# Optimization experiments

Measured on AMD Instinct MI355X. Metric: run time of the kernel, lower is better.

## Reference

```python
import jax, jax.numpy as jnp
import numpy as np

# model constants
D = 2048; D_INNER = 4096; H = 64; P = 64; N = 128; K = 4; CHUNK = 256
E = 8; TOPK = 2; I_EXP = 1024; I_SH = 4096
EPS = 1e-5; RES_MULT = 0.22
CONV_DIM = D_INNER + 2 * N  # n_groups=1


def rmsnorm(x, w, eps=EPS):
    var = jnp.mean(x * x, axis=-1, keepdims=True)
    return x * jax.lax.rsqrt(var + eps) * w


def segsum(x):
    # x: [..., L] -> [..., L, L] lower-triangular cumulative sums, -inf above diag
    L = x.shape[-1]
    cs = jnp.cumsum(x, axis=-1)
    d = cs[..., :, None] - cs[..., None, :]
    mask = jnp.tril(jnp.ones((L, L), dtype=bool))
    return jnp.where(mask, d, -jnp.inf)


def ssd(x, dt, A, Bm, Cm, chunk=CHUNK):
    # x:[b,s,h,p] dt:[b,s,h] A:[h] Bm/Cm:[b,s,n] (single group)
    b, S, h, p = x.shape
    n = Bm.shape[-1]
    nc = S // chunk
    xc = x.reshape(b, nc, chunk, h, p)
    dtc = dt.reshape(b, nc, chunk, h)
    Bc = Bm.reshape(b, nc, chunk, n)
    Cc = Cm.reshape(b, nc, chunk, n)
    dA = jnp.transpose(dtc * A, (0, 1, 3, 2))          # [b,c,h,l]
    dA_cum = jnp.cumsum(dA, axis=-1)                    # [b,c,h,l]
    xdt = xc * dtc[..., None]                           # [b,c,l,h,p]
    # intra-chunk (quadratic attention-like block)
    CB = jnp.einsum('bcln,bcsn->bcls', Cc, Bc)
    Lmat = jnp.exp(segsum(dA))                          # [b,c,h,l,s]
    Y = jnp.einsum('bcls,bchls,bcshp->bclhp', CB, Lmat, xdt)
    # per-chunk final states
    decay_states = jnp.exp(dA_cum[..., -1:] - dA_cum)   # [b,c,h,l]
    states = jnp.einsum('bcln,bchl,bclhp->bchpn', Bc, decay_states, xdt)
    # inter-chunk recurrence (small scan over nc chunks)
    chunk_decay = jnp.exp(dA_cum[..., -1])              # [b,c,h]
    dec_c = jnp.moveaxis(chunk_decay, 1, 0)             # [c,b,h]
    st_c = jnp.moveaxis(states, 1, 0)                   # [c,b,h,p,n]

    def step(carry, inp):
        dec, st = inp
        return carry * dec[..., None, None] + st, carry

    _, prev = jax.lax.scan(step, jnp.zeros_like(st_c[0]), (dec_c, st_c))
    prev = jnp.moveaxis(prev, 0, 1)                     # [b,c,h,p,n] state before each chunk
    out_decay = jnp.exp(jnp.transpose(dA_cum, (0, 1, 3, 2)))  # [b,c,l,h]
    Y = Y + jnp.einsum('bcln,bchpn->bclhp', Cc, prev) * out_decay[..., None]
    return Y.reshape(b, S, h, p)


def causal_conv_silu(u, w, bias):
    # u:[b,s,c], depthwise causal conv kernel w:[c,K]
    S = u.shape[1]
    up = jnp.pad(u, ((0, 0), (K - 1, 0), (0, 0)))
    y = sum(up[:, i:i + S, :] * w[:, i] for i in range(K)) + bias
    return jax.nn.silu(y)


def setup_inputs() -> dict:
    key = jax.random.key(0)
    ks = jax.random.split(key, 16)
    B, S = 1, 4096
    sc = 0.02
    return {
        'positions': jnp.arange(B * S, dtype=jnp.int32).reshape(B, S),
        'hidden_states': jax.random.normal(ks[0], (B, S, D), jnp.float32),
        'ln1_w': jnp.ones((D,), jnp.float32),
        'in_proj_w': jax.random.normal(ks[1], (D, 2 * D_INNER + 2 * N + H), jnp.float32) * sc,
        'conv_w': jax.random.normal(ks[2], (CONV_DIM, K), jnp.float32) * 0.2,
        'conv_b': jnp.zeros((CONV_DIM,), jnp.float32),
        'A_log': jnp.log(jax.random.uniform(ks[3], (H,), jnp.float32, 1.0, 16.0)),
        'dt_bias': jax.random.normal(ks[4], (H,), jnp.float32) * 0.5,
        'D_param': jnp.ones((H,), jnp.float32),
        'mamba_norm_w': jnp.ones((D_INNER,), jnp.float32),
        'out_proj_w': jax.random.normal(ks[5], (D_INNER, D), jnp.float32) * sc,
        'ln2_w': jnp.ones((D,), jnp.float32),
        'router_w': jax.random.normal(ks[6], (D, E), jnp.float32) * sc,
        'moe_w_gate_up': jax.random.normal(ks[7], (E, D, 2 * I_EXP), jnp.float32) * sc,
        'moe_w_down': jax.random.normal(ks[8], (E, I_EXP, D), jnp.float32) * sc,
        'shared_w_in': jax.random.normal(ks[9], (D, 2 * I_SH), jnp.float32) * sc,
        'shared_w_out': jax.random.normal(ks[10], (I_SH, D), jnp.float32) * sc,
    }


def reference(positions, hidden_states, ln1_w, in_proj_w, conv_w, conv_b, A_log,
              dt_bias, D_param, mamba_norm_w, out_proj_w, ln2_w, router_w,
              moe_w_gate_up, moe_w_down, shared_w_in, shared_w_out):
    B, S, _ = hidden_states.shape
    residual = hidden_states
    h = rmsnorm(hidden_states, ln1_w)
    # ---- Mamba2 mixer ----
    proj = h @ in_proj_w                                  # [B,S,2*Di+2N+H]
    z = proj[..., :D_INNER]
    xBC = proj[..., D_INNER:D_INNER + CONV_DIM]
    dt_raw = proj[..., D_INNER + CONV_DIM:]
    xBC = causal_conv_silu(xBC, conv_w, conv_b)
    x = xBC[..., :D_INNER].reshape(B, S, H, P)
    Bm = xBC[..., D_INNER:D_INNER + N]
    Cm = xBC[..., D_INNER + N:]
    dt = jax.nn.softplus(dt_raw + dt_bias)                # [B,S,H]
    A = -jnp.exp(A_log)                                   # [H]
    y = ssd(x, dt, A, Bm, Cm) + x * D_param[None, None, :, None]
    y = y.reshape(B, S, D_INNER)
    y = rmsnorm(y * jax.nn.silu(z), mamba_norm_w)         # gated RMSNorm
    mamba_out = y @ out_proj_w
    hidden = residual + mamba_out * RES_MULT
    residual = hidden
    # ---- MoE + shared MLP ----
    h2 = rmsnorm(hidden, ln2_w)
    ht = h2.reshape(-1, D)
    T = ht.shape[0]
    logits = ht @ router_w                                # [T,E]
    topv, topi = jax.lax.top_k(logits, TOPK)
    wts = jax.nn.softmax(topv, axis=-1)
    gates = jnp.zeros((T, E), ht.dtype).at[jnp.arange(T)[:, None], topi].set(wts)
    moe_out = jnp.zeros_like(ht)
    for e in range(E):
        gu = ht @ moe_w_gate_up[e]
        a = jax.nn.silu(gu[:, :I_EXP]) * gu[:, I_EXP:]
        moe_out = moe_out + gates[:, e:e + 1] * (a @ moe_w_down[e])
    gu = ht @ shared_w_in
    shared_out = (jax.nn.silu(gu[:, :I_SH]) * gu[:, I_SH:]) @ shared_w_out
    ff = (moe_out + shared_out).reshape(B, S, D)
    hidden = residual + ff * RES_MULT
    return (hidden, residual)
```

## Files before the change

### kernel.cpp

```cpp
#include <hip/hip_runtime.h>
#include <stdint.h>

typedef unsigned short u16;
typedef __attribute__((ext_vector_type(8))) __bf16 bf16x8;
typedef __attribute__((ext_vector_type(4))) float f32x4;

#define SEQ     4096
#define DMODEL  2048
#define DINNER  4096
#define NHEADS  64
#define HEADP   64
#define NSTATE  128
#define NCHUNK  16
#define CHUNKL  256
#define NPROJ   8512
#define NPROJP  8576
#define CONVDIM 4352
#define RESM    0.22f
#define MAXROWS 9216
#define MAXTILE 72

static __device__ __forceinline__ u16 f2bf(float f){
  union { float f; uint32_t u; } v; v.f = f;
  uint32_t r = v.u + 0x7fffu + ((v.u >> 16) & 1u);
  return (u16)(r >> 16);
}
static __device__ __forceinline__ float bf2f(u16 h){
  union { uint32_t u; float f; } v; v.u = ((uint32_t)h) << 16;
  return v.f;
}
static __device__ __forceinline__ float siluf(float x){ return x / (1.f + __expf(-x)); }

static __device__ __forceinline__ void gll16(const void* g, void* l) {
  __builtin_amdgcn_global_load_lds(
      (const __attribute__((address_space(1))) void*)g,
      (__attribute__((address_space(3))) void*)l, 16, 0, 0);
}

static __device__ __forceinline__ int swz_src_c8(int tid) {
  return ((((tid & 3) - ((tid >> 3) & 3) + 4) & 3) * 8);
}
static __device__ __forceinline__ int swz_rd_sl8(int fr, int g) {
  return (((g + ((fr >> 1) & 3)) & 3) * 8);
}

static __device__ __forceinline__ void decode_tile(
    int id, int NB, int MB, int G, int& bx, int& by)
{
  const int nwg = NB * MB;
  int sid = id;
  if (!(nwg & 7)) {
    const int cpx = nwg >> 3;
    sid = (id & 7) * cpx + (id >> 3);
  }
  const int gsz = MB * G;
  const int fullG = NB / G;
  const int fullCnt = fullG * gsz;
  if (sid < fullCnt) {
    const int grp = sid / gsz;
    const int r = sid - grp * gsz;
    const int q = r / G;
    by = q;
    bx = grp * G + (r - q * G);
  } else {
    const int rem = NB - fullG * G;
    const int r = sid - fullCnt;
    const int q = r / rem;
    by = q;
    bx = fullG * G + (r - q * rem);
  }
}

__global__ __launch_bounds__(256) void rmsnorm_split(
    const float* __restrict__ in, const float* __restrict__ w,
    u16* __restrict__ hi, u16* __restrict__ lo, int width)
{
  const int row = blockIdx.x;
  const float* x = in + (size_t)row * width;
  float ss = 0.f;
  for (int i = threadIdx.x * 4; i < width; i += 1024) {
    float4 v = *(const float4*)&x[i];
    ss += v.x*v.x + v.y*v.y + v.z*v.z + v.w*v.w;
  }
  #pragma unroll
  for (int off = 32; off > 0; off >>= 1) ss += __shfl_down(ss, off);
  __shared__ float red[4];
  if ((threadIdx.x & 63) == 0) red[threadIdx.x >> 6] = ss;
  __syncthreads();
// ... 128 lines not shown
        Cf[(size_t)m * ldc + n] = acc[mi][ni][i];
      }
    }
  }
}

__global__ __launch_bounds__(256, 2) void gemm_bt_glu(
    const u16* __restrict__ A, const u16* __restrict__ Bt,
    u16* __restrict__ aout,
    int K, int Nhalf, int NB, int MB, int G)
{
  __shared__ u16 As[128 * 32];
  __shared__ u16 Bs[128 * 32];
  int bx, by; decode_tile(blockIdx.x, NB, MB, G, bx, by);
  const int tid = threadIdx.x, lane = tid & 63;
  const int wid = tid >> 6, wr = wid >> 1, wc = wid & 1;
  const int m0 = by * 128, n0 = bx * 128;
  const int fr = lane & 15, g = lane >> 4;
  const int sl8 = swz_rd_sl8(fr, g);
  const f32x4 zero = {0.f, 0.f, 0.f, 0.f};
  f32x4 acc[4][4];
  #pragma unroll
  for (int i = 0; i < 4; i++)
    #pragma unroll
    for (int j = 0; j < 4; j++) acc[i][j] = zero;
  const int c8 = swz_src_c8(tid);
  const u16* pA = A  + (size_t)(m0 + (tid >> 2)) * K + c8;
  const u16* pB = Bt + (size_t)(n0 + (tid >> 2)) * K + c8;
  const size_t rstep = (size_t)64 * K;
  const int l0 = tid * 8;
  for (int k0 = 0; k0 < K; k0 += 32) {
    if (k0) __syncthreads();
    gll16(pA + k0,         &As[l0]);
    gll16(pA + k0 + rstep, &As[2048 + l0]);
    gll16(pB + k0,         &Bs[l0]);
    gll16(pB + k0 + rstep, &Bs[2048 + l0]);
    __syncthreads();
    bf16x8 af[4], bfr[4];
    #pragma unroll
    for (int mi = 0; mi < 4; mi++)
      af[mi] = *(const bf16x8*)&As[(wr * 64 + mi * 16 + fr) * 32 + sl8];
    #pragma unroll
    for (int ni = 0; ni < 4; ni++)
      bfr[ni] = *(const bf16x8*)&Bs[(wc * 64 + ni * 16 + fr) * 32 + sl8];
    #pragma unroll
    for (int mi = 0; mi < 4; mi++)
      #pragma unroll
      for (int ni = 0; ni < 4; ni++)
        acc[mi][ni] = __builtin_amdgcn_mfma_f32_16x16x32_bf16(af[mi], bfr[ni], acc[mi][ni], 0, 0, 0);
  }
  #pragma unroll
  for (int mi = 0; mi < 4; mi++) {
    #pragma unroll
    for (int ni = 0; ni < 4; ni++) {
      const int n = n0 + wc * 64 + ni * 16 + fr;
      #pragma unroll
      for (int i = 0; i < 4; i++) {
        const float v = acc[mi][ni][i];
        const float vp = __shfl_xor(v, 1);
        if (!(fr & 1)) {
          const int m = m0 + wr * 64 + mi * 16 + g * 4 + i;
          aout[(size_t)m * Nhalf + (n >> 1)] = f2bf(siluf(v) * vp);
        }
      }
    }
  }
}

template<int EPI>
__global__ __launch_bounds__(256, 2) void gemm_dd(
    const u16* __restrict__ Ah, const u16* __restrict__ Al,
    const u16* __restrict__ Bh, const u16* __restrict__ Bl,
    float* __restrict__ Cf, const float* __restrict__ res,
    int Nreal, int K, int ldc, float alpha, int NB, int MB, int G)
{
  __shared__ u16 Ash[128 * 32];
  __shared__ u16 Asl[128 * 32];
  __shared__ u16 Bsh[128 * 32];
  __shared__ u16 Bsl[128 * 32];
  int bx, by; decode_tile(blockIdx.x, NB, MB, G, bx, by);
  const int tid = threadIdx.x, lane = tid & 63;
  const int wid = tid >> 6, wr = wid >> 1, wc = wid & 1;
  const int m0 = by * 128, n0 = bx * 128;
  const int fr = lane & 15, g = lane >> 4;
  const int sl8 = swz_rd_sl8(fr, g);
  const f32x4 zero = {0.f, 0.f, 0.f, 0.f};
  f32x4 acc[4][4];
  #pragma unroll
  for (int i = 0; i < 4; i++)
    #pragma unroll
    for (int j = 0; j < 4; j++) acc[i][j] = zero;
  const int c8 = swz_src_c8(tid);
  const size_t offA = (size_t)(m0 + (tid >> 2)) * K + c8;
  const size_t offB = (size_t)(n0 + (tid >> 2)) * K + c8;
  const size_t rstep = (size_t)64 * K;
  const int l0 = tid * 8;
  for (int k0 = 0; k0 < K; k0 += 32) {
    if (k0) __syncthreads();
    gll16(Ah + offA + k0,         &Ash[l0]);
    gll16(Ah + offA + k0 + rstep, &Ash[2048 + l0]);
    gll16(Al + offA + k0,         &Asl[l0]);
    gll16(Al + offA + k0 + rstep, &Asl[2048 + l0]);
    gll16(Bh + offB + k0,         &Bsh[l0]);
    gll16(Bh + offB + k0 + rstep, &Bsh[2048 + l0]);
    gll16(Bl + offB + k0,         &Bsl[l0]);
    gll16(Bl + offB + k0 + rstep, &Bsl[2048 + l0]);
    __syncthreads();
    bf16x8 ah[4], al[4], bh[4], bl[4];
    #pragma unroll
    for (int mi = 0; mi < 4; mi++) {
      const int a = (wr * 64 + mi * 16 + fr) * 32 + sl8;
      ah[mi] = *(const bf16x8*)&Ash[a];
      al[mi] = *(const bf16x8*)&Asl[a];
    }
    #pragma unroll
    for (int ni = 0; ni < 4; ni++) {
      const int b = (wc * 64 + ni * 16 + fr) * 32 + sl8;
      bh[ni] = *(const bf16x8*)&Bsh[b];
      bl[ni] = *(const bf16x8*)&Bsl[b];
    }
    #pragma unroll
    for (int mi = 0; mi < 4; mi++)
      #pragma unroll
      for (int ni = 0; ni < 4; ni++) {
        acc[mi][ni] = __builtin_amdgcn_mfma_f32_16x16x32_bf16(al[mi], bh[ni], acc[mi][ni], 0, 0, 0);
        acc[mi][ni] = __builtin_amdgcn_mfma_f32_16x16x32_bf16(ah[mi], bl[ni], acc[mi][ni], 0, 0, 0);
        acc[mi][ni] = __builtin_amdgcn_mfma_f32_16x16x32_bf16(ah[mi], bh[ni], acc[mi][ni], 0, 0, 0);
      }
  }
  #pragma unroll
  for (int mi = 0; mi < 4; mi++) {
    #pragma unroll
    for (int ni = 0; ni < 4; ni++) {
      const int n = n0 + wc * 64 + ni * 16 + fr;
      if (n >= Nreal) continue;
      #pragma unroll
      for (int i = 0; i < 4; i++) {
        const int m = m0 + wr * 64 + mi * 16 + g * 4 + i;
        const float v = acc[mi][ni][i];
        const size_t idx = (size_t)m * ldc + n;
        if constexpr (EPI == 1) {
          Cf[idx] = res[idx] + alpha * v;
        } else {
          Cf[idx] = v;
        }
      }
    }
  }
}

__global__ __launch_bounds__(256, 2) void gemm_moe_gu(
    const u16* __restrict__ ht, const u16* __restrict__ wGU,
    u16* __restrict__ abufp, const int* __restrict__ tokmap,
    const int* __restrict__ meta)
{
  const int by = blockIdx.y;
  if (by >= meta[24]) return;
  const int e = meta[32 + by];
  const int row0 = meta[104 + by];
  __shared__ u16 As[128 * 32];
  __shared__ u16 Bs[128 * 32];
  const int tid = threadIdx.x, lane = tid & 63;
  const int wid = tid >> 6, wr = wid >> 1, wc = wid & 1;
  const int n0 = blockIdx.x * 128;
  const int fr = lane & 15, g = lane >> 4;
  const int sl8 = swz_rd_sl8(fr, g);
  const f32x4 zero = {0.f, 0.f, 0.f, 0.f};
  f32x4 acc[4][4];
  #pragma unroll
  for (int i = 0; i < 4; i++)
    #pragma unroll
    for (int j = 0; j < 4; j++) acc[i][j] = zero;
  const int r4 = tid >> 2, c8 = swz_src_c8(tid);
  const int tok0 = tokmap[row0 + r4];
  const int tok1 = tokmap[row0 + 64 + r4];
  const u16* pA0 = ht + (size_t)tok0 * DMODEL + c8;
  const u16* pA1 = ht + (size_t)tok1 * DMODEL + c8;
  const u16* pB  = wGU + (size_t)e * 2048 * DMODEL + (size_t)(n0 + r4) * DMODEL + c8;
  const size_t rstep = (size_t)64 * DMODEL;
  const int l0 = tid * 8;
  for (int k0 = 0; k0 < DMODEL; k0 += 32) {
    if (k0) __syncthreads();
    gll16(pA0 + k0,        &As[l0]);
    gll16(pA1 + k0,        &As[2048 + l0]);
    gll16(pB + k0,         &Bs[l0]);
    gll16(pB + k0 + rstep, &Bs[2048 + l0]);
    __syncthreads();
    bf16x8 af[4], bfr[4];
    #pragma unroll
    for (int mi = 0; mi < 4; mi++)
      af[mi] = *(const bf16x8*)&As[(wr * 64 + mi * 16 + fr) * 32 + sl8];
    #pragma unroll
    for (int ni = 0; ni < 4; ni++)
      bfr[ni] = *(const bf16x8*)&Bs[(wc * 64 + ni * 16 + fr) * 32 + sl8];
    #pragma unroll
    for (int mi = 0; mi < 4; mi++)
      #pragma unroll
      for (int ni = 0; ni < 4; ni++)
        acc[mi][ni] = __builtin_amdgcn_mfma_f32_16x16x32_bf16(af[mi], bfr[ni], acc[mi][ni], 0, 0, 0);
  }
  #pragma unroll
  for (int mi = 0; mi < 4; mi++)
    #pragma unroll
    for (int ni = 0; ni < 4; ni++) {
      const int n = n0 + wc * 64 + ni * 16 + fr;
      #pragma unroll
      for (int i = 0; i < 4; i++) {
        const float v = acc[mi][ni][i];
        const float vp = __shfl_xor(v, 1);
        if (!(fr & 1)) {
          const int m = row0 + wr * 64 + mi * 16 + g * 4 + i;
          abufp[(size_t)m * 1024 + (n >> 1)] = f2bf(siluf(v) * vp);
        }
      }
    }
}

__global__ __launch_bounds__(256, 2) void gemm_moe_down(
    const u16* __restrict__ abuf, const u16* __restrict__ wDN,
    u16* __restrict__ dout, const float* __restrict__ gatew,
    const int* __restrict__ meta)
{
  const int by = blockIdx.y;
  if (by >= meta[24]) return;
  const int e = meta[32 + by];
  const int row0 = meta[104 + by];
  __shared__ u16 As[128 * 32];
  __shared__ u16 Bs[128 * 32];
  const int tid = threadIdx.x, lane = tid & 63;
  const int wid = tid >> 6, wr = wid >> 1, wc = wid & 1;
  const int n0 = blockIdx.x * 128;
// ... 45 lines not shown

__global__ __launch_bounds__(256) void conv_silu_dt(
    const float* __restrict__ proj, const float* __restrict__ cw, const float* __restrict__ cb,
    const float* __restrict__ dt_bias,
    float* __restrict__ x, float* __restrict__ Bc, float* __restrict__ Cc,
    float* __restrict__ dt)
{
  const int c = blockIdx.x * 256 + threadIdx.x;
  const int s = blockIdx.y;
  if (c < CONVDIM) {
    const float4 w = *(const float4*)&cw[c * 4];
    float acc = cb[c];
    const float* pc = proj + (size_t)DINNER + c;
    if (s >= 3) acc += pc[(size_t)(s-3) * NPROJP] * w.x;
    if (s >= 2) acc += pc[(size_t)(s-2) * NPROJP] * w.y;
    if (s >= 1) acc += pc[(size_t)(s-1) * NPROJP] * w.z;
    acc += pc[(size_t)s * NPROJP] * w.w;
    const float v = siluf(acc);
    if (c < DINNER)                 x[(size_t)s * DINNER + c] = v;
    else if (c < DINNER + NSTATE)   Bc[(size_t)s * NSTATE + (c - DINNER)] = v;
    else                            Cc[(size_t)s * NSTATE + (c - DINNER - NSTATE)] = v;
  } else if (c < CONVDIM + 64) {
    const int h = c - CONVDIM;
    const float v = proj[(size_t)s * NPROJP + (DINNER + CONVDIM) + h] + dt_bias[h];
    dt[(size_t)s * 64 + h] = fmaxf(v, 0.f) + log1pf(__expf(-fabsf(v)));
  }
}

__global__ __launch_bounds__(64) void ssd_cum_seq(
    const float* __restrict__ dt, const float* __restrict__ A_log,
    float* __restrict__ cum, float* __restrict__ cdec)
{
  const int c = blockIdx.x, h = threadIdx.x;
  const float A = -__expf(A_log[h]);
  float run = 0.f;
  float* co = cum + ((size_t)(c * 64 + h)) * 256;
  const float* dp = dt + (size_t)c * 256 * 64 + h;
  #pragma unroll 4
  for (int l = 0; l < 256; l++) {
    run += dp[(size_t)l * 64] * A;
    co[l] = run;
  }
  cdec[c * 64 + h] = __expf(run);
}

__global__ __launch_bounds__(256) void ssd_cb(
    const float* __restrict__ Cc, const float* __restrict__ Bc, float* __restrict__ CBt)
{
  const int c = blockIdx.y;
  const int lt = blockIdx.x >> 2, st = blockIdx.x & 3;
  if (st > lt) return;
  __shared__ float Cn[128][64];
  __shared__ float Bn[128][64];
  const int tid = threadIdx.x;
  #pragma unroll
  for (int rep = 0; rep < 8; rep++) {
    const int lin = rep * 1024 + tid * 4;
    const int r = lin >> 7, cc = lin & 127;
    float4 cv = *(const float4*)&Cc[((size_t)(c*256 + lt*64 + r)) * 128 + cc];
    float4 bv = *(const float4*)&Bc[((size_t)(c*256 + st*64 + r)) * 128 + cc];
    Cn[cc+0][r] = cv.x; Cn[cc+1][r] = cv.y; Cn[cc+2][r] = cv.z; Cn[cc+3][r] = cv.w;
    Bn[cc+0][r] = bv.x; Bn[cc+1][r] = bv.y; Bn[cc+2][r] = bv.z; Bn[cc+3][r] = bv.w;
  }
  __syncthreads();
  const int lb = (tid >> 4) * 4, sb = (tid & 15) * 4;
  float acc[4][4] = {};
  for (int n = 0; n < 128; n++) {
    float cv[4], bv[4];
    #pragma unroll
    for (int i = 0; i < 4; i++) { cv[i] = Cn[n][lb+i]; bv[i] = Bn[n][sb+i]; }
    #pragma unroll
    for (int i = 0; i < 4; i++)
      #pragma unroll
      for (int j = 0; j < 4; j++) acc[i][j] += cv[i] * bv[j];
  }
  #pragma unroll
  for (int is = 0; is < 4; is++) {
    const int sg = st*64 + sb + is;
    float4 o; o.x = acc[0][is]; o.y = acc[1][is]; o.z = acc[2][is]; o.w = acc[3][is];
    *(float4*)&CBt[((size_t)(c*256 + sg)) * 256 + lt*64 + lb] = o;
  }
}

__global__ __launch_bounds__(256, 2) void ssd_intra_mfma(
    const float* __restrict__ x, const float* __restrict__ dt, const float* __restrict__ cum,
    const float* __restrict__ CBt, float* __restrict__ Yw)
{
  const int c = blockIdx.x, h = blockIdx.y;
  const int tid = threadIdx.x, lane = tid & 63, w = tid >> 6;
  const int fr = lane & 15, g = lane >> 4;
  __shared__ float cumL[256];
  __shared__ u16 Ph[256 * 32], Pl[256 * 32];
  __shared__ u16 Xh[64 * 32],  Xl[64 * 32];
  cumL[tid] = cum[((size_t)(c*64 + h)) * 256 + tid];
  const f32x4 zero = {0.f, 0.f, 0.f, 0.f};
  f32x4 acc[4][4];
  #pragma unroll
  for (int i = 0; i < 4; i++)
    #pragma unroll
    for (int j = 0; j < 4; j++) acc[i][j] = zero;
  const size_t cb0 = (size_t)c * 65536;
  for (int ts = 0; ts < 8; ts++) {
    __syncthreads();
    {
      const int sl = tid >> 3, p0 = (tid & 7) * 8;
      const int sg = c*256 + ts*32 + sl;
      const float dtv = dt[(size_t)sg * 64 + h];
      const float* xr = x + (size_t)sg * DINNER + h*64 + p0;
      const float4 v0 = *(const float4*)&xr[0];
      const float4 v1 = *(const float4*)&xr[4];
      #pragma unroll
      for (int q = 0; q < 8; q++) {
        const float v = ((q < 4) ? ((const float*)&v0)[q] : ((const float*)&v1)[q-4]) * dtv;
        const u16 H = f2bf(v);
        Xh[(p0 + q) * 32 + sl] = H;
        Xl[(p0 + q) * 32 + sl] = f2bf(v - bf2f(H));
      }
    }
    {
      const int l = tid;
      const float myc = cumL[l];
      #pragma unroll 4
      for (int j = 0; j < 32; j++) {
        const int s = ts*32 + j;
        const float cb = CBt[cb0 + (size_t)s * 256 + l];
        float p = 0.f;
        if (s <= l) p = cb * __expf(myc - cumL[s]);
        const u16 H = f2bf(p);
        Ph[l * 32 + j] = H;
        Pl[l * 32 + j] = f2bf(p - bf2f(H));
      }
    }
    __syncthreads();
    if (ts * 32 < (w + 1) * 64) {
      bf16x8 ah[4], al[4], bh[4], bl[4];
      #pragma unroll
      for (int mi = 0; mi < 4; mi++) {
        const int a = (w*64 + mi*16 + fr) * 32 + g*8;
        ah[mi] = *(const bf16x8*)&Ph[a];
        al[mi] = *(const bf16x8*)&Pl[a];
      }
      #pragma unroll
      for (int ni = 0; ni < 4; ni++) {
        const int b = (ni*16 + fr) * 32 + g*8;
        bh[ni] = *(const bf16x8*)&Xh[b];
        bl[ni] = *(const bf16x8*)&Xl[b];
      }
      #pragma unroll
      for (int mi = 0; mi < 4; mi++)
        #pragma unroll
        for (int ni = 0; ni < 4; ni++) {
          acc[mi][ni] = __builtin_amdgcn_mfma_f32_16x16x32_bf16(al[mi], bh[ni], acc[mi][ni], 0, 0, 0);
          acc[mi][ni] = __builtin_amdgcn_mfma_f32_16x16x32_bf16(ah[mi], bl[ni], acc[mi][ni], 0, 0, 0);
          acc[mi][ni] = __builtin_amdgcn_mfma_f32_16x16x32_bf16(ah[mi], bh[ni], acc[mi][ni], 0, 0, 0);
        }
    }
  }
  #pragma unroll
  for (int mi = 0; mi < 4; mi++)
    #pragma unroll
    for (int ni = 0; ni < 4; ni++)
      #pragma unroll
      for (int i = 0; i < 4; i++) {
        const int l = w*64 + mi*16 + g*4 + i;
        const int p = ni*16 + fr;
        Yw[(size_t)(c*256 + l) * DINNER + h*64 + p] = acc[mi][ni][i];
      }
}

__global__ __launch_bounds__(256, 2) void ssd_states_mfma(
    const float* __restrict__ x, const float* __restrict__ Bc, const float* __restrict__ dt,
    const float* __restrict__ cum, float* __restrict__ states)
{
  const int c = blockIdx.x, h = blockIdx.y;
  const int tid = threadIdx.x, lane = tid & 63, w = tid >> 6;
  const int fr = lane & 15, g = lane >> 4;
  __shared__ float cd[256];
  __shared__ u16 Xth[64 * 32],  Xtl[64 * 32];
  __shared__ u16 Bth[128 * 32], Btl[128 * 32];
  {
    const float* cumh = cum + ((size_t)(c*64 + h)) * 256;
    cd[tid] = __expf(cumh[255] - cumh[tid]) * dt[(size_t)(c*256 + tid) * 64 + h];
  }
  const f32x4 zero = {0.f, 0.f, 0.f, 0.f};
  f32x4 acc[4][2];
  #pragma unroll
  for (int i = 0; i < 4; i++) { acc[i][0] = zero; acc[i][1] = zero; }
  for (int lt = 0; lt < 8; lt++) {
    __syncthreads();
    {
      const int ll = tid >> 3, p0 = (tid & 7) * 8;
      const int lg = c*256 + lt*32 + ll;
      const float cdv = cd[lt*32 + ll];
      const float* xr = x + (size_t)lg * DINNER + h*64 + p0;
      const float4 v0 = *(const float4*)&xr[0];
      const float4 v1 = *(const float4*)&xr[4];
      #pragma unroll
      for (int q = 0; q < 8; q++) {
        const float v = ((q < 4) ? ((const float*)&v0)[q] : ((const float*)&v1)[q-4]) * cdv;
        const u16 H = f2bf(v);
        Xth[(p0 + q) * 32 + ll] = H;
        Xtl[(p0 + q) * 32 + ll] = f2bf(v - bf2f(H));
      }
    }
    {
      const int ll = tid >> 3, n0 = (tid & 7) * 16;
      const float* br = Bc + (size_t)(c*256 + lt*32 + ll) * 128 + n0;
      #pragma unroll
      for (int q4 = 0; q4 < 4; q4++) {
        const float4 bv = *(const float4*)&br[q4*4];
        #pragma unroll
        for (int q = 0; q < 4; q++) {
          const float v = ((const float*)&bv)[q];
          const u16 H = f2bf(v);
          Bth[(n0 + q4*4 + q) * 32 + ll] = H;
          Btl[(n0 + q4*4 + q) * 32 + ll] = f2bf(v - bf2f(H));
        }
      }
    }
    __syncthreads();
    bf16x8 ah[4], al[4], bh[2], bl[2];
    #pragma unroll
    for (int mi = 0; mi < 4; mi++) {
      const int a = (mi*16 + fr) * 32 + g*8;
      ah[mi] = *(const bf16x8*)&Xth[a];
      al[mi] = *(const bf16x8*)&Xtl[a];
    }
    #pragma unroll
    for (int ni = 0; ni < 2; ni++) {
      const int b = (w*32 + ni*16 + fr) * 32 + g*8;
      bh[ni] = *(const bf16x8*)&Bth[b];
      bl[ni] = *(const bf16x8*)&Btl[b];
    }
    #pragma unroll
    for (int mi = 0; mi < 4; mi++)
      #pragma unroll
      for (int ni = 0; ni < 2; ni++) {
        acc[mi][ni] = __builtin_amdgcn_mfma_f32_16x16x32_bf16(al[mi], bh[ni], acc[mi][ni], 0, 0, 0);
        acc[mi][ni] = __builtin_amdgcn_mfma_f32_16x16x32_bf16(ah[mi], bl[ni], acc[mi][ni], 0, 0, 0);
        acc[mi][ni] = __builtin_amdgcn_mfma_f32_16x16x32_bf16(ah[mi], bh[ni], acc[mi][ni], 0, 0, 0);
      }
  }
  #pragma unroll
  for (int mi = 0; mi < 4; mi++)
    #pragma unroll
    for (int ni = 0; ni < 2; ni++)
      #pragma unroll
      for (int i = 0; i < 4; i++) {
        const int p = mi*16 + g*4 + i;
        const int n = w*32 + ni*16 + fr;
        states[(((size_t)(c*64 + h)) * 64 + p) * 128 + n] = acc[mi][ni][i];
      }
}

__global__ void ssd_scan(
    const float* __restrict__ states, const float* __restrict__ cdec, float* __restrict__ prev)
{
  const int hp = blockIdx.x;
  const int n = threadIdx.x;
  const int h = hp >> 6;
  float carry = 0.f;
  for (int c = 0; c < NCHUNK; c++) {
    const size_t idx = ((size_t)c * 4096 + hp) * 128 + n;
    prev[idx] = carry;
    carry = carry * cdec[c*64 + h] + states[idx];
  }
}

__global__ __launch_bounds__(256, 2) void ssd_final_mfma(
    const float* __restrict__ Cc, const float* __restrict__ prev, const float* __restrict__ cum,
    const float* __restrict__ x, const float* __restrict__ proj, const float* __restrict__ Dp,
    float* __restrict__ Yw)
{
  const int c = blockIdx.x, h = blockIdx.y;
  const int tid = threadIdx.x, lane = tid & 63, w = tid >> 6;
  const int fr = lane & 15, g = lane >> 4;
  __shared__ float cumL[256];
  __shared__ u16 Ch[256 * 32], Cl[256 * 32];
  __shared__ u16 Pvh[64 * 32], Pvl[64 * 32];
  cumL[tid] = cum[((size_t)(c*64 + h)) * 256 + tid];
  const f32x4 zero = {0.f, 0.f, 0.f, 0.f};
  f32x4 acc[4][4];
  #pragma unroll
  for (int i = 0; i < 4; i++)
    #pragma unroll
    for (int j = 0; j < 4; j++) acc[i][j] = zero;
  for (int nt = 0; nt < 4; nt++) {
    __syncthreads();
    {
      #pragma unroll
      for (int rep = 0; rep < 32; rep++) {
        const int l = rep*8 + (tid >> 5);
        const int j = tid & 31;
        const float v = Cc[(size_t)(c*256 + l) * 128 + nt*32 + j];
        const u16 H = f2bf(v);
        Ch[l*32 + j] = H;
        Cl[l*32 + j] = f2bf(v - bf2f(H));
      }
    }
    {
      const int p = tid >> 2, q0 = (tid & 3) * 8;
      const float* pr = prev + ((size_t)c * 4096 + h*64 + p) * 128 + nt*32 + q0;
      const float4 v0 = *(const float4*)&pr[0];
      const float4 v1 = *(const float4*)&pr[4];
      #pragma unroll
      for (int q = 0; q < 8; q++) {
        const float v = (q < 4) ? ((const float*)&v0)[q] : ((const float*)&v1)[q-4];
        const u16 H = f2bf(v);
        Pvh[p*32 + q0 + q] = H;
        Pvl[p*32 + q0 + q] = f2bf(v - bf2f(H));
      }
    }
    __syncthreads();
    bf16x8 ah[4], al[4], bh[4], bl[4];
    #pragma unroll
    for (int mi = 0; mi < 4; mi++) {
      const int a = (w*64 + mi*16 + fr) * 32 + g*8;
      ah[mi] = *(const bf16x8*)&Ch[a];
      al[mi] = *(const bf16x8*)&Cl[a];
    }
    #pragma unroll
    for (int ni = 0; ni < 4; ni++) {
      const int b = (ni*16 + fr) * 32 + g*8;
      bh[ni] = *(const bf16x8*)&Pvh[b];
      bl[ni] = *(const bf16x8*)&Pvl[b];
    }
    #pragma unroll
    for (int mi = 0; mi < 4; mi++)
      #pragma unroll
      for (int ni = 0; ni < 4; ni++) {
        acc[mi][ni] = __builtin_amdgcn_mfma_f32_16x16x32_bf16(al[mi], bh[ni], acc[mi][ni], 0, 0, 0);
        acc[mi][ni] = __builtin_amdgcn_mfma_f32_16x16x32_bf16(ah[mi], bl[ni], acc[mi][ni], 0, 0, 0);
        acc[mi][ni] = __builtin_amdgcn_mfma_f32_16x16x32_bf16(ah[mi], bh[ni], acc[mi][ni], 0, 0, 0);
      }
  }
  const float Dv = Dp[h];
  #pragma unroll
  for (int mi = 0; mi < 4; mi++) {
    #pragma unroll
    for (int i = 0; i < 4; i++) {
      const int l = w*64 + mi*16 + g*4 + i;
      const float odec = __expf(cumL[l]);
      const size_t rowo = (size_t)(c*256 + l);
      #pragma unroll
      for (int ni = 0; ni < 4; ni++) {
        const int p = ni*16 + fr;
        const size_t iy = rowo * DINNER + h*64 + p;
        const float yv = Yw[iy] + acc[mi][ni][i] * odec + Dv * x[iy];
        const float z = proj[rowo * NPROJP + h*64 + p];
        Yw[iy] = yv * siluf(z);
      }
    }
  }
}

__global__ __launch_bounds__(256) void router_norm(
    const float* __restrict__ h2, const float* __restrict__ ln2w,
    const float* __restrict__ rw, u16* __restrict__ ht,
    int* __restrict__ eidx, float* __restrict__ ew)
{
  const int t = blockIdx.x;
  const float* xr = h2 + (size_t)t * DMODEL;
  float ss = 0.f;
  for (int i = threadIdx.x * 4; i < DMODEL; i += 1024) {
    float4 v = *(const float4*)&xr[i];
    ss += v.x*v.x + v.y*v.y + v.z*v.z + v.w*v.w;
  }
  #pragma unroll
  for (int off = 32; off > 0; off >>= 1) ss += __shfl_down(ss, off);
  __shared__ float red[4];
  if ((threadIdx.x & 63) == 0) red[threadIdx.x >> 6] = ss;
  __syncthreads();
  const float scale = rsqrtf((red[0]+red[1]+red[2]+red[3]) / (float)DMODEL + 1e-5f);
  float acc[8];
  #pragma unroll
  for (int j = 0; j < 8; j++) acc[j] = 0.f;
  u16* o = ht + (size_t)t * DMODEL;
  for (int i = threadIdx.x; i < DMODEL; i += 256) {
    const float v = xr[i] * scale * ln2w[i];
    o[i] = f2bf(v);
    const float* r = rw + (size_t)i * 8;
    #pragma unroll
    for (int j = 0; j < 8; j++) acc[j] += v * r[j];
  }
  #pragma unroll
  for (int j = 0; j < 8; j++)
    #pragma unroll
    for (int off = 32; off > 0; off >>= 1) acc[j] += __shfl_down(acc[j], off);
  __shared__ float rbuf[4][8];
  if ((threadIdx.x & 63) == 0)
    #pragma unroll
    for (int j = 0; j < 8; j++) rbuf[threadIdx.x >> 6][j] = acc[j];
  __syncthreads();
  if (threadIdx.x == 0) {
    float lg[8];
    #pragma unroll
    for (int j = 0; j < 8; j++) lg[j] = rbuf[0][j]+rbuf[1][j]+rbuf[2][j]+rbuf[3][j];
    int i1 = 0;
    #pragma unroll
    for (int j = 1; j < 8; j++) if (lg[j] > lg[i1]) i1 = j;
    int i2 = -1;
    #pragma unroll
    for (int j = 0; j < 8; j++) if (j != i1 && (i2 < 0 || lg[j] > lg[i2])) i2 = j;
    const float e2 = __expf(lg[i2] - lg[i1]);
    const float inv = 1.f / (1.f + e2);
    eidx[t*2]   = i1;  ew[t*2]   = inv;
    eidx[t*2+1] = i2;  ew[t*2+1] = e2 * inv;
  }
}

__global__ __launch_bounds__(1024) void moe_route(
    const int* __restrict__ eidx, const float* __restrict__ ew,
    int* __restrict__ tokmap, float* __restrict__ gatew,
    int* __restrict__ posmap, int* __restrict__ meta)
{
  const int tid = threadIdx.x;
  __shared__ int cnt[8], base[8];
  if (tid < 8) cnt[tid] = 0;
  for (int i = tid; i < MAXROWS; i += 1024) tokmap[i] = 0;
  __syncthreads();
  for (int i = tid; i < SEQ * 2; i += 1024)
    atomicAdd(&cnt[eidx[i]], 1);
  __syncthreads();
  if (tid == 0) {
    int off = 0, T = 0;
    for (int e = 0; e < 8; e++) {
      base[e] = off;
      meta[16 + e] = off;
      const int nt = (cnt[e] + 127) >> 7;
      for (int j = 0; j < nt; j++) {
        meta[32 + T] = e;
// ... 36 lines not shown
#define OFF_WAH   ((size_t)0)
#define OFF_WAL   ((size_t)35127296)
#define OFF_PROJ  ((size_t)70254592)
#define OFF_X     ((size_t)210763776)
#define OFF_Y     ((size_t)277872640)
#define OFF_HP    ((size_t)344981504)
#define OFF_BC    ((size_t)378535936)
#define OFF_CC    ((size_t)380633088)
#define OFF_DT    ((size_t)382730240)
#define OFF_CUM   ((size_t)383778816)
#define OFF_CDEC  ((size_t)384827392)
#define OFF_CB    ((size_t)384831488)

extern "C" void kernel_launch(void* const* d_in, const int* in_sizes, int n_in,
                              void* d_out, int out_size, void* d_ws, size_t ws_size,
                              hipStream_t stream)
{
  const float* hs       = (const float*)d_in[1];
  const float* ln1_w    = (const float*)d_in[2];
  const float* w_inproj = (const float*)d_in[3];
  const float* conv_w   = (const float*)d_in[4];
  const float* conv_b   = (const float*)d_in[5];
  const float* A_log    = (const float*)d_in[6];
  const float* dt_bias  = (const float*)d_in[7];
  const float* D_param  = (const float*)d_in[8];
  const float* mnorm_w  = (const float*)d_in[9];
  const float* w_outp   = (const float*)d_in[10];
  const float* ln2_w    = (const float*)d_in[11];
  const float* router_w = (const float*)d_in[12];
  const float* w_gu     = (const float*)d_in[13];
  const float* w_down   = (const float*)d_in[14];
  const float* w_shin   = (const float*)d_in[15];
  const float* w_shout  = (const float*)d_in[16];

  char* ws = (char*)d_ws;
  u16*   wAh    = (u16*)(ws + OFF_WAH);
  u16*   wAl    = (u16*)(ws + OFF_WAL);
  float* projf  = (float*)(ws + OFF_PROJ);
  float* xbuf   = (float*)(ws + OFF_X);
  float* ybuf   = (float*)(ws + OFF_Y);
  float* Bcb    = (float*)(ws + OFF_BC);
  float* Ccb    = (float*)(ws + OFF_CC);
  float* dtb    = (float*)(ws + OFF_DT);
  float* cumb   = (float*)(ws + OFF_CUM);
  float* cdecb  = (float*)(ws + OFF_CDEC);
  float* cbt    = (float*)(ws + OFF_CB);

  u16*   hhi    = (u16*)(ws + OFF_HP);
  u16*   hlo    = (u16*)(ws + OFF_HP + 16777216);
  float* prevb  = (float*)(ws + OFF_HP);
  u16*   wDN    = (u16*)(ws + OFF_HP);
  float* stbuf  = (float*)(ws + OFF_WAH);
  u16*   ynhi   = (u16*)(ws + OFF_WAH);
  u16*   ynlo   = (u16*)(ws + OFF_WAL);
  u16*   wBh    = (u16*)(ws + OFF_PROJ);
  u16*   wBl    = (u16*)(ws + OFF_PROJ + 16777216);
  u16*   wE     = (u16*)(ws + OFF_WAH);
  u16*   wD     = (u16*)(ws + OFF_WAH + 33554432);
  u16*   wGU    = (u16*)(ws + OFF_WAH);
  u16*   abufp  = (u16*)(ws + OFF_PROJ + 83886080);
  u16*   ht     = (u16*)(ws + OFF_X);
  u16*   ash    = (u16*)(ws + OFF_X + 16777216);
  u16*   dout   = (u16*)(ws + OFF_X + 16777216);
  float* shout  = (float*)(ws + OFF_Y);

  int*   eidx   = (int*)(ws + OFF_BC);
  float* ew     = (float*)(ws + OFF_BC + 65536);
  int*   posmap = (int*)(ws + OFF_BC + 131072);
  int*   tokmap = (int*)(ws + OFF_BC + 196608);
  float* gatew  = (float*)(ws + OFF_BC + 262144);
  int*   meta   = (int*)(ws + OFF_BC + 327680);

  float* out0    = (float*)d_out;
  float* hidden2 = out0 + (size_t)SEQ * DMODEL;

  rmsnorm_split<<<SEQ, 256, 0, stream>>>(hs, ln1_w, hhi, hlo, DMODEL);
  wconv_t_split<<<dim3(NPROJ/32, DMODEL/32), 256, 0, stream>>>(w_inproj, wAh, wAl, DMODEL, NPROJ);
  gemm_dd<3><<<67*32, 256, 0, stream>>>(hhi, hlo, wAh, wAl, projf, nullptr,
                                        NPROJ, DMODEL, NPROJP, 0.f, 67, 32, 4);
  conv_silu_dt<<<dim3(18, SEQ), 256, 0, stream>>>(projf, conv_w, conv_b, dt_bias,
                                                  xbuf, Bcb, Ccb, dtb);
  ssd_cum_seq<<<NCHUNK, 64, 0, stream>>>(dtb, A_log, cumb, cdecb);
  ssd_cb<<<dim3(16, NCHUNK), 256, 0, stream>>>(Ccb, Bcb, cbt);
  ssd_intra_mfma<<<dim3(NCHUNK, NHEADS), 256, 0, stream>>>(xbuf, dtb, cumb, cbt, ybuf);
  ssd_states_mfma<<<dim3(NCHUNK, NHEADS), 256, 0, stream>>>(xbuf, Bcb, dtb, cumb, stbuf);
  ssd_scan<<<NHEADS*HEADP, 128, 0, stream>>>(stbuf, cdecb, prevb);
  ssd_final_mfma<<<dim3(NCHUNK, NHEADS), 256, 0, stream>>>(Ccb, prevb, cumb, xbuf, projf, D_param, ybuf);
  rmsnorm_split<<<SEQ, 256, 0, stream>>>(ybuf, mnorm_w, ynhi, ynlo, DINNER);
  wconv_t_split<<<dim3(DMODEL/32, DINNER/32), 256, 0, stream>>>(w_outp, wBh, wBl, DINNER, DMODEL);
  gemm_dd<1><<<16*32, 256, 0, stream>>>(ynhi, ynlo, wBh, wBl, hidden2, hs,
                                        DMODEL, DINNER, DMODEL, RESM, 16, 32, 4);

  router_norm<<<SEQ, 256, 0, stream>>>(hidden2, ln2_w, router_w, ht, eidx, ew);
  moe_route<<<1, 1024, 0, stream>>>(eidx, ew, tokmap, gatew, posmap, meta);

  wconv_t_glu<<<dim3(8192/32, DMODEL/32), 256, 0, stream>>>(w_shin, wE, DMODEL, 8192, 4096);
  gemm_bt_glu<<<64*32, 256, 0, stream>>>(ht, wE, ash, DMODEL, 4096, 64, 32, 4);
  wconv_t<<<dim3(DMODEL/32, 4096/32), 256, 0, stream>>>(w_shout, wD, 4096, DMODEL);
  gemm_bt<3><<<16*32, 256, 0, stream>>>(ash, wD, shout, DMODEL, 4096, DMODEL, 16, 32, 4);

  wconv_t_glu<<<dim3(2048/32, DMODEL/32, 8), 256, 0, stream>>>(w_gu, wGU, DMODEL, 2048, 1024);
  wconv_t<<<dim3(DMODEL/32, 1024/32, 8), 256, 0, stream>>>(w_down, wDN, 1024, DMODEL);
  gemm_moe_gu<<<dim3(16, MAXTILE), 256, 0, stream>>>(ht, wGU, abufp, tokmap, meta);
  gemm_moe_down<<<dim3(16, MAXTILE), 256, 0, stream>>>(abufp, wDN, dout, gatew, meta);

  final_moe<<<SEQ, 256, 0, stream>>>(hidden2, shout, dout, posmap, out0);
}
```

Before: 1.729 ms.

## Fuse SSD intra-chunk and final kernels; switch split-bf16 GEMM to 32x32 MFMA

```diff
diff --git a/kernel.cpp b/kernel.cpp
--- a/kernel.cpp
+++ b/kernel.cpp
@@ -4,6 +4,7 @@
 typedef unsigned short u16;
 typedef __attribute__((ext_vector_type(8))) __bf16 bf16x8;
 typedef __attribute__((ext_vector_type(4))) float f32x4;
+typedef __attribute__((ext_vector_type(16))) float f32x16;
 
 #define SEQ     4096
 #define DMODEL  2048
@@ -298,14 +299,15 @@
   const int tid = threadIdx.x, lane = tid & 63;
   const int wid = tid >> 6, wr = wid >> 1, wc = wid & 1;
   const int m0 = by * 128, n0 = bx * 128;
-  const int fr = lane & 15, g = lane >> 4;
-  const int sl8 = swz_rd_sl8(fr, g);
-  const f32x4 zero = {0.f, 0.f, 0.f, 0.f};
-  f32x4 acc[4][4];
-  #pragma unroll
-  for (int i = 0; i < 4; i++)
-    #pragma unroll
-    for (int j = 0; j < 4; j++) acc[i][j] = zero;
+  const int r32 = lane & 31, kg = lane >> 5;
+  const int sbase = (r32 >> 1) & 3;
+  f32x16 acc[2][2];
+  #pragma unroll
+  for (int i = 0; i < 2; i++)
+    #pragma unroll
+    for (int j = 0; j < 2; j++)
+      #pragma unroll
+      for (int q = 0; q < 16; q++) acc[i][j][q] = 0.f;
   const int c8 = swz_src_c8(tid);
   const size_t offA = (size_t)(m0 + (tid >> 2)) * K + c8;
   const size_t offB = (size_t)(n0 + (tid >> 2)) * K + c8;
@@ -322,38 +324,46 @@
     gll16(Bl + offB + k0,         &Bsl[l0]);
     gll16(Bl + offB + k0 + rstep, &Bsl[2048 + l0]);
     __syncthreads();
-    bf16x8 ah[4], al[4], bh[4], bl[4];
-    #pragma unroll
-    for (int mi = 0; mi < 4; mi++) {
-      const int a = (wr * 64 + mi * 16 + fr) * 32 + sl8;
-      ah[mi] = *(const bf16x8*)&Ash[a];
-      al[mi] = *(const bf16x8*)&Asl[a];
-    }
-    #pragma unroll
-    for (int ni = 0; ni < 4; ni++) {
-      const int b = (wc * 64 + ni * 16 + fr) * 32 + sl8;
-      bh[ni] = *(const bf16x8*)&Bsh[b];
-      bl[ni] = *(const bf16x8*)&Bsl[b];
-    }
-    #pragma unroll
-    for (int mi = 0; mi < 4; mi++)
-      #pragma unroll
-      for (int ni = 0; ni < 4; ni++) {
-        acc[mi][ni] = __builtin_amdgcn_mfma_f32_16x16x32_bf16(al[mi], bh[ni], acc[mi][ni], 0, 0, 0);
-        acc[mi][ni] = __builtin_amdgcn_mfma_f32_16x16x32_bf16(ah[mi], bl[ni], acc[mi][ni], 0, 0, 0);
-        acc[mi][ni] = __builtin_amdgcn_mfma_f32_16x16x32_bf16(ah[mi], bh[ni], acc[mi][ni], 0, 0, 0);
-      }
-  }
-  #pragma unroll
-  for (int mi = 0; mi < 4; mi++) {
-    #pragma unroll
-    for (int ni = 0; ni < 4; ni++) {
-      const int n = n0 + wc * 64 + ni * 16 + fr;
+    bf16x8 ah[2][2], al[2][2], bh[2][2], bl[2][2];
+    #pragma unroll
+    for (int at = 0; at < 2; at++)
+      #pragma unroll
+      for (int ks = 0; ks < 2; ks++) {
+        const int row = wr * 64 + at * 32 + r32;
+        const int a = row * 32 + (((ks * 2 + kg) + sbase) & 3) * 8;
+        ah[at][ks] = *(const bf16x8*)&Ash[a];
+        al[at][ks] = *(const bf16x8*)&Asl[a];
+      }
+    #pragma unroll
+    for (int bt = 0; bt < 2; bt++)
+      #pragma unroll
+      for (int ks = 0; ks < 2; ks++) {
+        const int row = wc * 64 + bt * 32 + r32;
+        const int b = row * 32 + (((ks * 2 + kg) + sbase) & 3) * 8;
+        bh[bt][ks] = *(const bf16x8*)&Bsh[b];
+        bl[bt][ks] = *(const bf16x8*)&Bsl[b];
+      }
+    #pragma unroll
+    for (int at = 0; at < 2; at++)
+      #pragma unroll
+      for (int bt = 0; bt < 2; bt++)
+        #pragma unroll
+        for (int ks = 0; ks < 2; ks++) {
+          acc[at][bt] = __builtin_amdgcn_mfma_f32_32x32x16_bf16(al[at][ks], bh[bt][ks], acc[at][bt], 0, 0, 0);
+          acc[at][bt] = __builtin_amdgcn_mfma_f32_32x32x16_bf16(ah[at][ks], bl[bt][ks], acc[at][bt], 0, 0, 0);
+          acc[at][bt] = __builtin_amdgcn_mfma_f32_32x32x16_bf16(ah[at][ks], bh[bt][ks], acc[at][bt], 0, 0, 0);
+        }
+  }
+  #pragma unroll
+  for (int at = 0; at < 2; at++)
+    #pragma unroll
+    for (int bt = 0; bt < 2; bt++) {
+      const int n = n0 + wc * 64 + bt * 32 + r32;
       if (n >= Nreal) continue;
       #pragma unroll
-      for (int i = 0; i < 4; i++) {
-        const int m = m0 + wr * 64 + mi * 16 + g * 4 + i;
-        const float v = acc[mi][ni][i];
+      for (int r = 0; r < 16; r++) {
+        const int m = m0 + wr * 64 + at * 32 + (r & 3) + 8 * (r >> 2) + 4 * kg;
+        const float v = acc[at][bt][r];
         const size_t idx = (size_t)m * ldc + n;
         if constexpr (EPI == 1) {
           Cf[idx] = res[idx] + alpha * v;
@@ -362,7 +372,6 @@
         }
       }
     }
-  }
 }
 
 __global__ __launch_bounds__(256, 2) void gemm_moe_gu(
@@ -574,17 +583,119 @@
   }
 }
 
-__global__ __launch_bounds__(256, 2) void ssd_intra_mfma(
+__global__ __launch_bounds__(256, 2) void ssd_states_mfma(
+    const float* __restrict__ x, const float* __restrict__ Bc, const float* __restrict__ dt,
+    const float* __restrict__ cum, float* __restrict__ states)
+{
+  const int c = blockIdx.x, h = blockIdx.y;
+  const int tid = threadIdx.x, lane = tid & 63, w = tid >> 6;
+  const int fr = lane & 15, g = lane >> 4;
+  __shared__ float cd[256];
+  __shared__ u16 Xth[64 * 32],  Xtl[64 * 32];
+  __shared__ u16 Bth[128 * 32], Btl[128 * 32];
+  {
+    const float* cumh = cum + ((size_t)(c*64 + h)) * 256;
+    cd[tid] = __expf(cumh[255] - cumh[tid]) * dt[(size_t)(c*256 + tid) * 64 + h];
+  }
+  const f32x4 zero = {0.f, 0.f, 0.f, 0.f};
+  f32x4 acc[4][2];
+  #pragma unroll
+  for (int i = 0; i < 4; i++) { acc[i][0] = zero; acc[i][1] = zero; }
+  for (int lt = 0; lt < 8; lt++) {
+    __syncthreads();
+    {
+      const int ll = tid >> 3, p0 = (tid & 7) * 8;
+      const int lg = c*256 + lt*32 + ll;
+      const float cdv = cd[lt*32 + ll];
+      const float* xr = x + (size_t)lg * DINNER + h*64 + p0;
+      const float4 v0 = *(const float4*)&xr[0];
+      const float4 v1 = *(const float4*)&xr[4];
+      #pragma unroll
+      for (int q = 0; q < 8; q++) {
+        const float v = ((q < 4) ? ((const float*)&v0)[q] : ((const float*)&v1)[q-4]) * cdv;
+        const u16 H = f2bf(v);
+        Xth[(p0 + q) * 32 + ll] = H;
+        Xtl[(p0 + q) * 32 + ll] = f2bf(v - bf2f(H));
+      }
+    }
+    {
+      const int ll = tid >> 3, n0 = (tid & 7) * 16;
+      const float* br = Bc + (size_t)(c*256 + lt*32 + ll) * 128 + n0;
+      #pragma unroll
+      for (int q4 = 0; q4 < 4; q4++) {
+        const float4 bv = *(const float4*)&br[q4*4];
+        #pragma unroll
+        for (int q = 0; q < 4; q++) {
+          const float v = ((const float*)&bv)[q];
+          const u16 H = f2bf(v);
+          Bth[(n0 + q4*4 + q) * 32 + ll] = H;
+          Btl[(n0 + q4*4 + q) * 32 + ll] = f2bf(v - bf2f(H));
+        }
+      }
+    }
+    __syncthreads();
+    bf16x8 ah[4], al[4], bh[2], bl[2];
+    #pragma unroll
+    for (int mi = 0; mi < 4; mi++) {
+      const int a = (mi*16 + fr) * 32 + g*8;
+      ah[mi] = *(const bf16x8*)&Xth[a];
+      al[mi] = *(const bf16x8*)&Xtl[a];
+    }
+    #pragma unroll
+    for (int ni = 0; ni < 2; ni++) {
+      const int b = (w*32 + ni*16 + fr) * 32 + g*8;
+      bh[ni] = *(const bf16x8*)&Bth[b];
+      bl[ni] = *(const bf16x8*)&Btl[b];
+    }
+    #pragma unroll
+    for (int mi = 0; mi < 4; mi++)
+      #pragma unroll
+      for (int ni = 0; ni < 2; ni++) {
+        acc[mi][ni] = __builtin_amdgcn_mfma_f32_16x16x32_bf16(al[mi], bh[ni], acc[mi][ni], 0, 0, 0);
+        acc[mi][ni] = __builtin_amdgcn_mfma_f32_16x16x32_bf16(ah[mi], bl[ni], acc[mi][ni], 0, 0, 0);
+        acc[mi][ni] = __builtin_amdgcn_mfma_f32_16x16x32_bf16(ah[mi], bh[ni], acc[mi][ni], 0, 0, 0);
+      }
+  }
+  #pragma unroll
+  for (int mi = 0; mi < 4; mi++)
+    #pragma unroll
+    for (int ni = 0; ni < 2; ni++)
+      #pragma unroll
+      for (int i = 0; i < 4; i++) {
+        const int p = mi*16 + g*4 + i;
+        const int n = w*32 + ni*16 + fr;
+        states[(((size_t)(c*64 + h)) * 64 + p) * 128 + n] = acc[mi][ni][i];
+      }
+}
+
+__global__ void ssd_scan(
+    const float* __restrict__ states, const float* __restrict__ cdec, float* __restrict__ prev)
+{
+  const int hp = blockIdx.x;
+  const int n = threadIdx.x;
+  const int h = hp >> 6;
+  float carry = 0.f;
+  for (int c = 0; c < NCHUNK; c++) {
+    const size_t idx = ((size_t)c * 4096 + hp) * 128 + n;
+    prev[idx] = carry;
+    carry = carry * cdec[c*64 + h] + states[idx];
+  }
+}
+
+__global__ __launch_bounds__(256, 2) void ssd_intra_final_mfma(
     const float* __restrict__ x, const float* __restrict__ dt, const float* __restrict__ cum,
-    const float* __restrict__ CBt, float* __restrict__ Yw)
+    const float* __restrict__ CBt, const float* __restrict__ Cc, const float* __restrict__ prev,
+    const float* __restrict__ proj, const float* __restrict__ Dp, float* __restrict__ Yw)
 {
   const int c = blockIdx.x, h = blockIdx.y;
   const int tid = threadIdx.x, lane = tid & 63, w = tid >> 6;
   const int fr = lane & 15, g = lane >> 4;
   __shared__ float cumL[256];
+  __shared__ float odecL[256];
   __shared__ u16 Ph[256 * 32], Pl[256 * 32];
   __shared__ u16 Xh[64 * 32],  Xl[64 * 32];
   cumL[tid] = cum[((size_t)(c*64 + h)) * 256 + tid];
+  odecL[tid] = __expf(cumL[tid]);
   const f32x4 zero = {0.f, 0.f, 0.f, 0.f};
   f32x4 acc[4][4];
   #pragma unroll
@@ -648,135 +759,6 @@
         }
     }
   }
-  #pragma unroll
-  for (int mi = 0; mi < 4; mi++)
-    #pragma unroll
-    for (int ni = 0; ni < 4; ni++)
-      #pragma unroll
-      for (int i = 0; i < 4; i++) {
-        const int l = w*64 + mi*16 + g*4 + i;
-        const int p = ni*16 + fr;
-        Yw[(size_t)(c*256 + l) * DINNER + h*64 + p] = acc[mi][ni][i];
-      }
-}
-
-__global__ __launch_bounds__(256, 2) void ssd_states_mfma(
-    const float* __restrict__ x, const float* __restrict__ Bc, const float* __restrict__ dt,
-    const float* __restrict__ cum, float* __restrict__ states)
-{
-  const int c = blockIdx.x, h = blockIdx.y;
-  const int tid = threadIdx.x, lane = tid & 63, w = tid >> 6;
-  const int fr = lane & 15, g = lane >> 4;
-  __shared__ float cd[256];
-  __shared__ u16 Xth[64 * 32],  Xtl[64 * 32];
-  __shared__ u16 Bth[128 * 32], Btl[128 * 32];
-  {
-    const float* cumh = cum + ((size_t)(c*64 + h)) * 256;
-    cd[tid] = __expf(cumh[255] - cumh[tid]) * dt[(size_t)(c*256 + tid) * 64 + h];
-  }
-  const f32x4 zero = {0.f, 0.f, 0.f, 0.f};
-  f32x4 acc[4][2];
-  #pragma unroll
-  for (int i = 0; i < 4; i++) { acc[i][0] = zero; acc[i][1] = zero; }
-  for (int lt = 0; lt < 8; lt++) {
-    __syncthreads();
-    {
-      const int ll = tid >> 3, p0 = (tid & 7) * 8;
-      const int lg = c*256 + lt*32 + ll;
-      const float cdv = cd[lt*32 + ll];
-      const float* xr = x + (size_t)lg * DINNER + h*64 + p0;
-      const float4 v0 = *(const float4*)&xr[0];
-      const float4 v1 = *(const float4*)&xr[4];
-      #pragma unroll
-      for (int q = 0; q < 8; q++) {
-        const float v = ((q < 4) ? ((const float*)&v0)[q] : ((const float*)&v1)[q-4]) * cdv;
-        const u16 H = f2bf(v);
-        Xth[(p0 + q) * 32 + ll] = H;
-        Xtl[(p0 + q) * 32 + ll] = f2bf(v - bf2f(H));
-      }
-    }
-    {
-      const int ll = tid >> 3, n0 = (tid & 7) * 16;
-      const float* br = Bc + (size_t)(c*256 + lt*32 + ll) * 128 + n0;
-      #pragma unroll
-      for (int q4 = 0; q4 < 4; q4++) {
-        const float4 bv = *(const float4*)&br[q4*4];
-        #pragma unroll
-        for (int q = 0; q < 4; q++) {
-          const float v = ((const float*)&bv)[q];
-          const u16 H = f2bf(v);
-          Bth[(n0 + q4*4 + q) * 32 + ll] = H;
-          Btl[(n0 + q4*4 + q) * 32 + ll] = f2bf(v - bf2f(H));
-        }
-      }
-    }
-    __syncthreads();
-    bf16x8 ah[4], al[4], bh[2], bl[2];
-    #pragma unroll
-    for (int mi = 0; mi < 4; mi++) {
-      const int a = (mi*16 + fr) * 32 + g*8;
-      ah[mi] = *(const bf16x8*)&Xth[a];
-      al[mi] = *(const bf16x8*)&Xtl[a];
-    }
-    #pragma unroll
-    for (int ni = 0; ni < 2; ni++) {
-      const int b = (w*32 + ni*16 + fr) * 32 + g*8;
-      bh[ni] = *(const bf16x8*)&Bth[b];
-      bl[ni] = *(const bf16x8*)&Btl[b];
-    }
-    #pragma unroll
-    for (int mi = 0; mi < 4; mi++)
-      #pragma unroll
-      for (int ni = 0; ni < 2; ni++) {
-        acc[mi][ni] = __builtin_amdgcn_mfma_f32_16x16x32_bf16(al[mi], bh[ni], acc[mi][ni], 0, 0, 0);
-        acc[mi][ni] = __builtin_amdgcn_mfma_f32_16x16x32_bf16(ah[mi], bl[ni], acc[mi][ni], 0, 0, 0);
-        acc[mi][ni] = __builtin_amdgcn_mfma_f32_16x16x32_bf16(ah[mi], bh[ni], acc[mi][ni], 0, 0, 0);
-      }
-  }
-  #pragma unroll
-  for (int mi = 0; mi < 4; mi++)
-    #pragma unroll
-    for (int ni = 0; ni < 2; ni++)
-      #pragma unroll
-      for (int i = 0; i < 4; i++) {
-        const int p = mi*16 + g*4 + i;
-        const int n = w*32 + ni*16 + fr;
-        states[(((size_t)(c*64 + h)) * 64 + p) * 128 + n] = acc[mi][ni][i];
-      }
-}
-
-__global__ void ssd_scan(
-    const float* __restrict__ states, const float* __restrict__ cdec, float* __restrict__ prev)
-{
-  const int hp = blockIdx.x;
-  const int n = threadIdx.x;
-  const int h = hp >> 6;
-  float carry = 0.f;
-  for (int c = 0; c < NCHUNK; c++) {
-    const size_t idx = ((size_t)c * 4096 + hp) * 128 + n;
-    prev[idx] = carry;
-    carry = carry * cdec[c*64 + h] + states[idx];
-  }
-}
-
-__global__ __launch_bounds__(256, 2) void ssd_final_mfma(
-    const float* __restrict__ Cc, const float* __restrict__ prev, const float* __restrict__ cum,
-    const float* __restrict__ x, const float* __restrict__ proj, const float* __restrict__ Dp,
-    float* __restrict__ Yw)
-{
-  const int c = blockIdx.x, h = blockIdx.y;
-  const int tid = threadIdx.x, lane = tid & 63, w = tid >> 6;
-  const int fr = lane & 15, g = lane >> 4;
-  __shared__ float cumL[256];
-  __shared__ u16 Ch[256 * 32], Cl[256 * 32];
-  __shared__ u16 Pvh[64 * 32], Pvl[64 * 32];
-  cumL[tid] = cum[((size_t)(c*64 + h)) * 256 + tid];
-  const f32x4 zero = {0.f, 0.f, 0.f, 0.f};
-  f32x4 acc[4][4];
-  #pragma unroll
-  for (int i = 0; i < 4; i++)
-    #pragma unroll
-    for (int j = 0; j < 4; j++) acc[i][j] = zero;
   for (int nt = 0; nt < 4; nt++) {
     __syncthreads();
     {
@@ -784,10 +766,10 @@
       for (int rep = 0; rep < 32; rep++) {
         const int l = rep*8 + (tid >> 5);
         const int j = tid & 31;
-        const float v = Cc[(size_t)(c*256 + l) * 128 + nt*32 + j];
+        const float v = Cc[(size_t)(c*256 + l) * 128 + nt*32 + j] * odecL[l];
         const u16 H = f2bf(v);
-        Ch[l*32 + j] = H;
-        Cl[l*32 + j] = f2bf(v - bf2f(H));
+        Ph[l*32 + j] = H;
+        Pl[l*32 + j] = f2bf(v - bf2f(H));
       }
     }
     {
@@ -799,8 +781,8 @@
       for (int q = 0; q < 8; q++) {
         const float v = (q < 4) ? ((const float*)&v0)[q] : ((const float*)&v1)[q-4];
         const u16 H = f2bf(v);
-        Pvh[p*32 + q0 + q] = H;
-        Pvl[p*32 + q0 + q] = f2bf(v - bf2f(H));
+        Xh[p*32 + q0 + q] = H;
+        Xl[p*32 + q0 + q] = f2bf(v - bf2f(H));
       }
     }
     __syncthreads();
@@ -808,14 +790,14 @@
     #pragma unroll
     for (int mi = 0; mi < 4; mi++) {
       const int a = (w*64 + mi*16 + fr) * 32 + g*8;
-      ah[mi] = *(const bf16x8*)&Ch[a];
-      al[mi] = *(const bf16x8*)&Cl[a];
+      ah[mi] = *(const bf16x8*)&Ph[a];
+      al[mi] = *(const bf16x8*)&Pl[a];
     }
     #pragma unroll
     for (int ni = 0; ni < 4; ni++) {
       const int b = (ni*16 + fr) * 32 + g*8;
-      bh[ni] = *(const bf16x8*)&Pvh[b];
-      bl[ni] = *(const bf16x8*)&Pvl[b];
+      bh[ni] = *(const bf16x8*)&Xh[b];
+      bl[ni] = *(const bf16x8*)&Xl[b];
     }
     #pragma unroll
     for (int mi = 0; mi < 4; mi++)
@@ -832,13 +814,12 @@
     #pragma unroll
     for (int i = 0; i < 4; i++) {
       const int l = w*64 + mi*16 + g*4 + i;
-      const float odec = __expf(cumL[l]);
       const size_t rowo = (size_t)(c*256 + l);
       #pragma unroll
       for (int ni = 0; ni < 4; ni++) {
         const int p = ni*16 + fr;
         const size_t iy = rowo * DINNER + h*64 + p;
-        const float yv = Yw[iy] + acc[mi][ni][i] * odec + Dv * x[iy];
+        const float yv = acc[mi][ni][i] + Dv * x[iy];
         const float z = proj[rowo * NPROJP + h*64 + p];
         Yw[iy] = yv * siluf(z);
       }
@@ -1041,10 +1022,10 @@
                                                   xbuf, Bcb, Ccb, dtb);
   ssd_cum_seq<<<NCHUNK, 64, 0, stream>>>(dtb, A_log, cumb, cdecb);
   ssd_cb<<<dim3(16, NCHUNK), 256, 0, stream>>>(Ccb, Bcb, cbt);
-  ssd_intra_mfma<<<dim3(NCHUNK, NHEADS), 256, 0, stream>>>(xbuf, dtb, cumb, cbt, ybuf);
   ssd_states_mfma<<<dim3(NCHUNK, NHEADS), 256, 0, stream>>>(xbuf, Bcb, dtb, cumb, stbuf);
   ssd_scan<<<NHEADS*HEADP, 128, 0, stream>>>(stbuf, cdecb, prevb);
-  ssd_final_mfma<<<dim3(NCHUNK, NHEADS), 256, 0, stream>>>(Ccb, prevb, cumb, xbuf, projf, D_param, ybuf);
+  ssd_intra_final_mfma<<<dim3(NCHUNK, NHEADS), 256, 0, stream>>>(
+      xbuf, dtb, cumb, cbt, Ccb, prevb, projf, D_param, ybuf);
   rmsnorm_split<<<SEQ, 256, 0, stream>>>(ybuf, mnorm_w, ynhi, ynlo, DINNER);
   wconv_t_split<<<dim3(DMODEL/32, DINNER/32), 256, 0, stream>>>(w_outp, wBh, wBl, DINNER, DMODEL);
   gemm_dd<1><<<16*32, 256, 0, stream>>>(ynhi, ynlo, wBh, wBl, hidden2, hs,
```

Result: slower. 1.837 ms (+6.2%).
